# Kernel optimization log

Measured on AMD Instinct MI355X. Metric: run time of the kernel, lower is better.

## Reference

```python
import jax, jax.numpy as jnp
import numpy as np

N, E, F, H, O, B = 100000, 1200000, 64, 1024, 1, 256


def _gcn_conv(x, W, b, src, dst, ew, num_nodes):
    # PyG GCNConv: out_i = sum_{(s->i)} d_i^{-1/2} w_e d_s^{-1/2} (x_s W) + b
    deg = jax.ops.segment_sum(ew, dst, num_segments=num_nodes)
    dinv = jnp.where(deg > 0, jax.lax.rsqrt(jnp.maximum(deg, 1e-12)), 0.0)
    norm = dinv[src] * ew * dinv[dst]          # [E]
    h = x @ W                                   # [N, out]
    msg = h[src] * norm[:, None]                # gather + scale
    return jax.ops.segment_sum(msg, dst, num_segments=num_nodes) + b


def setup_inputs() -> dict:
    key = jax.random.key(0)
    ks = jax.random.split(key, 12)
    def lin(k, fan_in, fan_out):
        s = 1.0 / np.sqrt(fan_in)
        kw, kb = jax.random.split(k)
        return (jax.random.uniform(kw, (fan_in, fan_out), jnp.float32, -s, s),
                jax.random.uniform(kb, (fan_out,), jnp.float32, -s, s))
    W1, b1 = lin(ks[0], F, F)
    W2, b2 = lin(ks[1], F, 2 * F)
    W3, b3 = lin(ks[2], 2 * F, 4 * F)
    Wf1, bf1 = lin(ks[3], 5 * F, H)
    Wf2, bf2 = lin(ks[4], H, O)
    feature = jax.random.normal(ks[5], (N, F), jnp.float32)
    edge_index = jax.random.randint(ks[6], (2, E), 0, N, jnp.int32)
    weight = jax.random.uniform(ks[7], (E,), jnp.float32)
    protein_batch = jnp.sort(jax.random.randint(ks[8], (N,), 0, B, jnp.int32))
    return {"feature": feature, "edge_index": edge_index, "weight": weight,
            "protein_batch": protein_batch,
            "W1": W1, "b1": b1, "W2": W2, "b2": b2, "W3": W3, "b3": b3,
            "Wf1": Wf1, "bf1": bf1, "Wf2": Wf2, "bf2": bf2}


def reference(feature, edge_index, weight, protein_batch,
              W1, b1, W2, b2, W3, b3, Wf1, bf1, Wf2, bf2):
    num_nodes = feature.shape[0]
    # add self-loops with weight 1 (PyG default)
    loop = jnp.arange(num_nodes, dtype=edge_index.dtype)
    src = jnp.concatenate([edge_index[0], loop])
    dst = jnp.concatenate([edge_index[1], loop])
    ew = jnp.concatenate([weight, jnp.ones((num_nodes,), weight.dtype)])

    x = jax.nn.relu(_gcn_conv(feature, W1, b1, src, dst, ew, num_nodes))
    x = jax.nn.relu(_gcn_conv(x, W2, b2, src, dst, ew, num_nodes))
    x = jax.nn.relu(_gcn_conv(x, W3, b3, src, dst, ew, num_nodes))
    x = jnp.concatenate([x, feature], axis=1)   # [N, 5F]

    # global_mean_pool over graph ids
    sums = jax.ops.segment_sum(x, protein_batch, num_segments=B)
    cnts = jax.ops.segment_sum(jnp.ones((num_nodes,), x.dtype), protein_batch, num_segments=B)
    gc = sums / jnp.maximum(cnts, 1.0)[:, None]

    gc = jax.nn.relu(gc @ Wf1 + bf1)            # dropout is identity in eval
    return gc @ Wf2 + bf2
```

## Files before the change

kernel.cpp:

```cpp
#include <hip/hip_runtime.h>
#include <cstdio>
#include <cstdint>

typedef _Float16 f16x8 __attribute__((ext_vector_type(8)));
typedef float f32x4 __attribute__((ext_vector_type(4)));

__device__ inline unsigned short f2bf(float f) {
  unsigned u = __float_as_uint(f);
  u += 0x7fffu + ((u >> 16) & 1u);
  return (unsigned short)(u >> 16);
}
__device__ inline float bf2f(unsigned short h) {
  return __uint_as_float(((unsigned)h) << 16);
}
__device__ inline unsigned short f2h(float f) {
  union { _Float16 h; unsigned short u; } cv;
  cv.h = (_Float16)f;
  return cv.u;
}

#define EPB 8192


__global__ __launch_bounds__(256)
void k_prep0(float* __restrict__ psum,
             const float* __restrict__ feature, ushort* __restrict__ featb,
             const float* __restrict__ W1, ushort* __restrict__ w1h,
             const float* __restrict__ W2, ushort* __restrict__ w2h,
             const float* __restrict__ W3, ushort* __restrict__ w3h,
             const int* __restrict__ pb, int* __restrict__ gs,
             const int* __restrict__ dst, int* __restrict__ H,
             int* __restrict__ rs,
             int BC, int NF, int F, int D2, int D3,
             int N, int B, int NB, int E,
             int nB, int nC, int nD, int nG) {
  __shared__ int hist[512];
  int b = blockIdx.x;
  int t = threadIdx.x;
  if (b < nB) {
    int i = b * 256 + t;
    if (i < BC) psum[i] = 0.f;
  } else if (b < nB + nC) {
    int base = ((b - nB) * 256 + t) * 4;
    if (base < NF) {
      float4 v = *reinterpret_cast<const float4*>(feature + base);
      ushort4 h;
      h.x = f2bf(v.x); h.y = f2bf(v.y); h.z = f2bf(v.z); h.w = f2bf(v.w);
      *reinterpret_cast<ushort4*>(featb + base) = h;
    }
  } else if (b < nB + nC + nD) {
    int idx = (b - nB - nC) * 256 + t;
    int s1 = F * F, s2 = s1 + F * D2, s3 = s2 + D2 * D3;
    if (idx < s1) {
      int k = idx / F, n = idx - k * F;
      w1h[(size_t)n * F + k] = f2h(W1[idx]);
    } else if (idx < s2) {
      int i2 = idx - s1; int k = i2 / D2, n = i2 - k * D2;
      w2h[(size_t)n * F + k] = f2h(W2[i2]);
    } else if (idx < s3) {
      int i3 = idx - s2; int k = i3 / D3, n = i3 - k * D3;
      w3h[(size_t)n * D2 + k] = f2h(W3[i3]);
    }
  } else if (b < nB + nC + nD + nG) {
    int bb = (b - nB - nC - nD) * 256 + t;
    if (bb == 0) rs[N] = E;
    if (bb <= B) {
      int lo = 0, hi = N;
      while (lo < hi) {
        int mid = (lo + hi) >> 1;
        if (pb[mid] < bb) lo = mid + 1; else hi = mid;
      }
      gs[bb] = lo;
    }
  } else {
    const int bi = b - nB - nC - nD - nG;
    for (int i = t; i < NB; i += 256) hist[i] = 0;
    __syncthreads();
    const int base = bi * EPB + t;
#pragma unroll
    for (int j = 0; j < EPB / 256; j++) {
      int e = base + 256 * j;
      if (e < E) atomicAdd(&hist[dst[e] >> 8], 1);
    }
    __syncthreads();
    for (int i = t; i < NB; i += 256) H[(size_t)bi * NB + i] = hist[i];
  }
}

__global__ __launch_bounds__(256)
void k_bscan1(const int* __restrict__ H, int* __restrict__ S,
              int* __restrict__ bsum, int NB, int NBLK, int T) {
  __shared__ int sh[256];
  const int t = threadIdx.x;
  const int base = blockIdx.x * 1024;
  int v[4]; int s = 0;
#pragma unroll
  for (int j = 0; j < 4; j++) {
    int idx = base + t * 4 + j;
    if (idx < T) {
      int bin = idx / NBLK, bi = idx - bin * NBLK;
      v[j] = H[(size_t)bi * NB + bin];
    } else v[j] = 0;
    s += v[j];
  }
  sh[t] = s;
  __syncthreads();
  for (int off = 1; off < 256; off <<= 1) {
    int x = (t >= off) ? sh[t - off] : 0;
    __syncthreads();
    sh[t] += x;
    __syncthreads();
  }
  int run = sh[t] - s;
#pragma unroll
  for (int j = 0; j < 4; j++) {
    int idx = base + t * 4 + j;
    if (idx < T) S[idx] = run;
    run += v[j];
  }
  if (t == 255) bsum[blockIdx.x] = sh[255];
}

__device__ inline void build_prefix(const int* __restrict__ bsum, int nch,
                                    int* __restrict__ pre, int t) {
  for (int i = t; i < nch; i += 256) pre[i] = bsum[i];
  __syncthreads();
  if (t == 0) {
    int run = 0;
    for (int i = 0; i < nch; i++) { int v = pre[i]; pre[i] = run; run += v; }
  }
  __syncthreads();
}

__global__ __launch_bounds__(256)
void k_bscatter(const int* __restrict__ src, const int* __restrict__ dst,
                const float* __restrict__ ew, const int* __restrict__ S,
                const int* __restrict__ bsb,
                int2* __restrict__ ssw,
                int NB, int NBLK, int E, int nchT) {
  __shared__ int cnt[512];
  __shared__ int sbase[512];
  __shared__ int pre[512];
  const int t = threadIdx.x, bi = blockIdx.x;
  build_prefix(bsb, nchT, pre, t);
  for (int i = t; i < NB; i += 256) {
    cnt[i] = 0;
    int j = i * NBLK + bi;
    sbase[i] = S[j] + pre[j >> 10];
  }
  __syncthreads();
  const int base = bi * EPB + t;
#pragma unroll
  for (int j = 0; j < EPB / 256; j++) {
    int e = base + 256 * j;
    if (e < E) {
      int d = dst[e];
      int bin = d >> 8;
      int r = atomicAdd(&cnt[bin], 1);
      int pos = sbase[bin] + r;
      ssw[pos] = make_int2(src[e] | ((d & 255) << 24), __float_as_int(ew[e]));
    }
  }
}

__global__ __launch_bounds__(256)
void k_bprocA(const int2* __restrict__ ssw,
              const int* __restrict__ S, const int* __restrict__ bsb,
              int* __restrict__ cntN, float* __restrict__ wsumN,
              int NB, int NBLK, int N, int E, int nchT) {
  __shared__ int cnt[256];
  __shared__ float wsm[256];
  __shared__ int pre[512];
  const int t = threadIdx.x, bin = blockIdx.x;
  build_prefix(bsb, nchT, pre, t);
  cnt[t] = 0; wsm[t] = 0.f;
  __syncthreads();
  int j0 = bin * NBLK;
  const int start = S[j0] + pre[j0 >> 10];
  int end = E;
  if (bin + 1 < NB) { int j1 = (bin + 1) * NBLK; end = S[j1] + pre[j1 >> 10]; }
  for (int p = start + t; p < end; p += 256) {
    int2 sw = ssw[p];
    int ld = (unsigned)sw.x >> 24;
    atomicAdd(&cnt[ld], 1);
    atomicAdd(&wsm[ld], __int_as_float(sw.y));
  }
  __syncthreads();
  int n = bin * 256 + t;
  if (n < N) { cntN[n] = cnt[t]; wsumN[n] = wsm[t]; }
}

__global__ __launch_bounds__(256)
void k_scan1(const int* __restrict__ cntN, const float* __restrict__ wsumN,
             int* __restrict__ rs, int* __restrict__ bsum,
             float* __restrict__ dinv, float* __restrict__ sn, int N) {
  __shared__ int sh[256];
  const int t = threadIdx.x;
  const int base = blockIdx.x * 1024;
  int v[4]; int s = 0;
#pragma unroll
  for (int j = 0; j < 4; j++) {
    int idx = base + t * 4 + j;
    if (idx < N) {
      v[j] = cntN[idx];
      double deg = 1.0 + (double)wsumN[idx];
      float r = (float)(1.0 / sqrt(deg));
      dinv[idx] = r;
      sn[idx] = r * r;
    } else v[j] = 0;
    s += v[j];
  }
  sh[t] = s;
  __syncthreads();
  for (int off = 1; off < 256; off <<= 1) {
    int x = (t >= off) ? sh[t - off] : 0;
    __syncthreads();
    sh[t] += x;
    __syncthreads();
  }
  int run = sh[t] - s;
#pragma unroll
  for (int j = 0; j < 4; j++) {
    int idx = base + t * 4 + j;
    if (idx < N) rs[idx] = run;
    run += v[j];
  }
  if (t == 255) bsum[blockIdx.x] = sh[255];
}

__global__ __launch_bounds__(256)
void k_bprocB(const int2* __restrict__ ssw,
              const int* __restrict__ S, const int* __restrict__ bsb,
              int* __restrict__ rs, const int* __restrict__ bsumN,
              const float* __restrict__ dinv,
              int2* __restrict__ epack,
              int NB, int NBLK, int N, int E, int nchT, int nchN) {
  __shared__ int cnt[256];
  __shared__ float sdv[256];
  __shared__ int srs[256];
  __shared__ int preT[512];
  __shared__ int preN[128];
  const int t = threadIdx.x, bin = blockIdx.x;
  for (int i = t; i < nchT; i += 256) preT[i] = bsb[i];
  for (int i = t; i < nchN; i += 256) preN[i] = bsumN[i];
  __syncthreads();
  if (t == 0) {
    int run = 0;
    for (int i = 0; i < nchT; i++) { int v = preT[i]; preT[i] = run; run += v; }
    run = 0;
    for (int i = 0; i < nchN; i++) { int v = preN[i]; preN[i] = run; run += v; }
  }
  __syncthreads();
  cnt[t] = 0;
  int n = bin * 256 + t;
  sdv[t] = (n < N) ? dinv[n] : 0.f;
  int rabs = 0;
  if (n < N) {
    rabs = rs[n] + preN[n >> 10];
    rs[n] = rabs;
  }
  srs[t] = rabs;
  __syncthreads();
  int j0 = bin * NBLK;
  const int start = S[j0] + preT[j0 >> 10];
  int end = E;
  if (bin + 1 < NB) { int j1 = (bin + 1) * NBLK; end = S[j1] + preT[j1 >> 10]; }
  for (int p = start + t; p < end; p += 256) {
    int2 sw = ssw[p];
    int ld = (unsigned)sw.x >> 24;
    int sidx = sw.x & 0x00FFFFFF;
    int r = atomicAdd(&cnt[ld], 1);
    float w = dinv[sidx] * __int_as_float(sw.y) * sdv[ld];
    epack[srs[ld] + r] = make_int2(sidx, __float_as_int(w));
  }
}


__device__ inline void bf8_fma(const int4 v, float w, float* acc) {
  acc[0] = fmaf(__uint_as_float((unsigned)v.x << 16), w, acc[0]);
  acc[1] = fmaf(__uint_as_float((unsigned)v.x & 0xffff0000u), w, acc[1]);
  acc[2] = fmaf(__uint_as_float((unsigned)v.y << 16), w, acc[2]);
  acc[3] = fmaf(__uint_as_float((unsigned)v.y & 0xffff0000u), w, acc[3]);
  acc[4] = fmaf(__uint_as_float((unsigned)v.z << 16), w, acc[4]);
  acc[5] = fmaf(__uint_as_float((unsigned)v.z & 0xffff0000u), w, acc[5]);
  acc[6] = fmaf(__uint_as_float((unsigned)v.w << 16), w, acc[6]);
  acc[7] = fmaf(__uint_as_float((unsigned)v.w & 0xffff0000u), w, acc[7]);
}

template<int LOG2L>
__global__ __launch_bounds__(256)
void k_aggregate_b(const ushort* __restrict__ Xb, const int* __restrict__ rs,
                   const int2* __restrict__ epack, const float* __restrict__ sn,
                   ushort* __restrict__ AH, int N) {
  const int t = blockIdx.x * blockDim.x + threadIdx.x;
  const int row = t >> LOG2L;
  if (row >= N) return;
  const int L = 1 << LOG2L;
  const int D = L << 3;
  const int c = (t & (L - 1)) << 3;
  const ushort* __restrict__ Xc = Xb + c;

  float acc[8];
  {
    int4 v = *reinterpret_cast<const int4*>(Xc + (size_t)row * D);
    float s = sn[row];
    acc[0] = s * __uint_as_float((unsigned)v.x << 16);
    acc[1] = s * __uint_as_float((unsigned)v.x & 0xffff0000u);
    acc[2] = s * __uint_as_float((unsigned)v.y << 16);
    acc[3] = s * __uint_as_float((unsigned)v.y & 0xffff0000u);
    acc[4] = s * __uint_as_float((unsigned)v.z << 16);
    acc[5] = s * __uint_as_float((unsigned)v.z & 0xffff0000u);
    acc[6] = s * __uint_as_float((unsigned)v.w << 16);
    acc[7] = s * __uint_as_float((unsigned)v.w & 0xffff0000u);
  }
  const int p0 = rs[row], pe = rs[row + 1];
  int i = p0;
  if ((i & 1) && i < pe) {
    int2 e = epack[i];
    int4 v = *reinterpret_cast<const int4*>(Xc + (size_t)e.x * D);
    bf8_fma(v, __int_as_float(e.y), acc);
    i++;
  }
  for (; i + 8 <= pe; i += 8) {
    int4 ea = *reinterpret_cast<const int4*>(&epack[i]);
    int4 eb = *reinterpret_cast<const int4*>(&epack[i + 2]);
    int4 ec = *reinterpret_cast<const int4*>(&epack[i + 4]);
    int4 ed = *reinterpret_cast<const int4*>(&epack[i + 6]);
    int4 v0 = *reinterpret_cast<const int4*>(Xc + (size_t)ea.x * D);
    int4 v1 = *reinterpret_cast<const int4*>(Xc + (size_t)ea.z * D);
    int4 v2 = *reinterpret_cast<const int4*>(Xc + (size_t)eb.x * D);
    int4 v3 = *reinterpret_cast<const int4*>(Xc + (size_t)eb.z * D);
    int4 v4 = *reinterpret_cast<const int4*>(Xc + (size_t)ec.x * D);
    int4 v5 = *reinterpret_cast<const int4*>(Xc + (size_t)ec.z * D);
    int4 v6 = *reinterpret_cast<const int4*>(Xc + (size_t)ed.x * D);
    int4 v7 = *reinterpret_cast<const int4*>(Xc + (size_t)ed.z * D);
    bf8_fma(v0, __int_as_float(ea.y), acc);
    bf8_fma(v1, __int_as_float(ea.w), acc);
    bf8_fma(v2, __int_as_float(eb.y), acc);
    bf8_fma(v3, __int_as_float(eb.w), acc);
    bf8_fma(v4, __int_as_float(ec.y), acc);
    bf8_fma(v5, __int_as_float(ec.w), acc);
    bf8_fma(v6, __int_as_float(ed.y), acc);
    bf8_fma(v7, __int_as_float(ed.w), acc);
  }
  if (i + 4 <= pe) {
    int4 ea = *reinterpret_cast<const int4*>(&epack[i]);
    int4 eb = *reinterpret_cast<const int4*>(&epack[i + 2]);
    int4 v0 = *reinterpret_cast<const int4*>(Xc + (size_t)ea.x * D);
    int4 v1 = *reinterpret_cast<const int4*>(Xc + (size_t)ea.z * D);
    int4 v2 = *reinterpret_cast<const int4*>(Xc + (size_t)eb.x * D);
    int4 v3 = *reinterpret_cast<const int4*>(Xc + (size_t)eb.z * D);
    bf8_fma(v0, __int_as_float(ea.y), acc);
    bf8_fma(v1, __int_as_float(ea.w), acc);
    bf8_fma(v2, __int_as_float(eb.y), acc);
    bf8_fma(v3, __int_as_float(eb.w), acc);
    i += 4;
  }
  if (i + 2 <= pe) {
    int4 e2 = *reinterpret_cast<const int4*>(&epack[i]);
    int4 v0 = *reinterpret_cast<const int4*>(Xc + (size_t)e2.x * D);
    int4 v1 = *reinterpret_cast<const int4*>(Xc + (size_t)e2.z * D);
    bf8_fma(v0, __int_as_float(e2.y), acc);
    bf8_fma(v1, __int_as_float(e2.w), acc);
    i += 2;
  }
  if (i < pe) {
    int2 e = epack[i];
    int4 v = *reinterpret_cast<const int4*>(Xc + (size_t)e.x * D);
    bf8_fma(v, __int_as_float(e.y), acc);
  }
  ushort h[8];
#pragma unroll
  for (int j = 0; j < 8; j++) h[j] = f2h(acc[j]);
  size_t o = (size_t)row * D + c;
  *reinterpret_cast<ushort4*>(AH + o)     = make_ushort4(h[0], h[1], h[2], h[3]);
  *reinterpret_cast<ushort4*>(AH + o + 4) = make_ushort4(h[4], h[5], h[6], h[7]);
}


template<int KT, int TPB>
__global__ __launch_bounds__(256, 3)
void k_gemm_rb(const ushort* __restrict__ Ah, const ushort* __restrict__ Bh,
               const float* __restrict__ bias, ushort* __restrict__ Y,
               int N, int D) {
  constexpr int NT = 64;
  constexpr int NK = KT / 32;
  const int t = threadIdx.x;
  const int wave = t >> 6, lane = t & 63;
  const int quad = lane >> 4, l16 = lane & 15;
  const int n0 = blockIdx.x * NT;
  const int mbase = blockIdx.y * (TPB * 128);

  f16x8 bf[NK][4];
#pragma unroll
  for (int k0 = 0; k0 < NK; k0++)
#pragma unroll
    for (int ni = 0; ni < 4; ni++)
      bf[k0][ni] = *reinterpret_cast<const f16x8*>(
          Bh + (size_t)(n0 + ni * 16 + l16) * KT + k0 * 32 + quad * 8);

  float bv[4];
#pragma unroll
  for (int ni = 0; ni < 4; ni++) bv[ni] = bias[n0 + ni * 16 + l16];

#pragma unroll 1
  for (int tile = 0; tile < TPB; tile++) {
    const int rt = mbase + tile * 128 + wave * 32 + l16;
    if (mbase + tile * 128 >= N) break;
    int r0 = rt;      if (r0 >= N) r0 = N - 1;
    int r1 = rt + 16; if (r1 >= N) r1 = N - 1;
    const ushort* __restrict__ A0 = Ah + (size_t)r0 * KT + quad * 8;
    const ushort* __restrict__ A1 = Ah + (size_t)r1 * KT + quad * 8;

    f16x8 a0[NK], a1[NK];
#pragma unroll
    for (int k0 = 0; k0 < NK; k0++) {
      a0[k0] = *reinterpret_cast<const f16x8*>(A0 + k0 * 32);
      a1[k0] = *reinterpret_cast<const f16x8*>(A1 + k0 * 32);
    }

    f32x4 acc[2][4];
#pragma unroll
    for (int mi = 0; mi < 2; mi++)
#pragma unroll
      for (int ni = 0; ni < 4; ni++) acc[mi][ni] = (f32x4){0.f, 0.f, 0.f, 0.f};

#pragma unroll
    for (int k0 = 0; k0 < NK; k0++)
#pragma unroll
      for (int ni = 0; ni < 4; ni++) {
        acc[0][ni] = __builtin_amdgcn_mfma_f32_16x16x32_f16(a0[k0], bf[k0][ni], acc[0][ni], 0, 0, 0);
        acc[1][ni] = __builtin_amdgcn_mfma_f32_16x16x32_f16(a1[k0], bf[k0][ni], acc[1][ni], 0, 0, 0);
      }

    const int rb0 = mbase + tile * 128 + wave * 32 + quad * 4;
#pragma unroll
    for (int mi = 0; mi < 2; mi++) {
      int rb = rb0 + mi * 16;
#pragma unroll
      for (int ni = 0; ni < 4; ni++) {
        int col = n0 + ni * 16 + l16;
#pragma unroll
        for (int r = 0; r < 4; r++) {
          int row = rb + r;
          if (row < N)
            Y[(size_t)row * D + col] = f2bf(fmaxf(acc[mi][ni][r] + bv[ni], 0.f));
        }
      }
    }
  }
}


#define PSPLIT 4

__global__ void k_pool(const ushort* __restrict__ X3b, const float* __restrict__ feat,
                       const int* __restrict__ gs, float* __restrict__ psum,
                       int D3, int F) {
  const int c = threadIdx.x;
  const int C = D3 + F;
  const int b = blockIdx.y;
  const int sp = blockIdx.x;
  const int s0 = gs[b], e0 = gs[b + 1];
  const int len = e0 - s0;
  if (len <= 0) return;
  const int chunk = (len + PSPLIT - 1) / PSPLIT;
  const int s = s0 + sp * chunk;
  int e = s + chunk; if (e > e0) e = e0;
  if (s >= e) return;
  const int n = e - s;
  float a0 = 0.f, a1 = 0.f, a2 = 0.f, a3 = 0.f;
  float a4 = 0.f, a5 = 0.f, a6 = 0.f, a7 = 0.f;
  if (c < D3) {
    const ushort* p = X3b + (size_t)s * D3 + c;
    int i = 0;
    for (; i + 8 <= n; i += 8) {
      a0 += bf2f(p[0 * (size_t)D3]);
      a1 += bf2f(p[1 * (size_t)D3]);
      a2 += bf2f(p[2 * (size_t)D3]);
      a3 += bf2f(p[3 * (size_t)D3]);
      a4 += bf2f(p[4 * (size_t)D3]);
      a5 += bf2f(p[5 * (size_t)D3]);
      a6 += bf2f(p[6 * (size_t)D3]);
      a7 += bf2f(p[7 * (size_t)D3]);
      p += 8 * (size_t)D3;
    }
    for (; i < n; i++) { a0 += bf2f(*p); p += D3; }
  } else {
    const float* p = feat + (size_t)s * F + (c - D3);
    int i = 0;
    for (; i + 8 <= n; i += 8) {
      a0 += p[0 * (size_t)F];
      a1 += p[1 * (size_t)F];
      a2 += p[2 * (size_t)F];
      a3 += p[3 * (size_t)F];
      a4 += p[4 * (size_t)F];
      a5 += p[5 * (size_t)F];
      a6 += p[6 * (size_t)F];
      a7 += p[7 * (size_t)F];
      p += 8 * (size_t)F;
    }
    for (; i < n; i++) { a0 += *p; p += F; }
  }
  float tot = ((a0 + a1) + (a2 + a3)) + ((a4 + a5) + (a6 + a7));
  atomicAdd(&psum[(size_t)b * C + c], tot);
}


__global__ __launch_bounds__(256)
void k_fc1(const float* __restrict__ psum, const int* __restrict__ gs,
           const float* __restrict__ Wf1, const float* __restrict__ bf1,
           float* __restrict__ hidden, int C, int Hh) {
  const int b = blockIdx.y;
  __shared__ float gcs[384];
  float invc = 1.f / fmaxf((float)(gs[b + 1] - gs[b]), 1.f);
  for (int c = threadIdx.x; c < C; c += 256)
    gcs[c] = psum[(size_t)b * C + c] * invc;
  __syncthreads();
  const int j = blockIdx.x * 256 + threadIdx.x;
  if (j >= Hh) return;
  const float* w = Wf1 + j;
  float a0 = 0.f, a1 = 0.f, a2 = 0.f, a3 = 0.f;
  int c = 0;
  for (; c + 4 <= C; c += 4) {
    a0 = fmaf(gcs[c + 0], w[(size_t)(c + 0) * Hh], a0);
    a1 = fmaf(gcs[c + 1], w[(size_t)(c + 1) * Hh], a1);
    a2 = fmaf(gcs[c + 2], w[(size_t)(c + 2) * Hh], a2);
    a3 = fmaf(gcs[c + 3], w[(size_t)(c + 3) * Hh], a3);
  }
  for (; c < C; c++) a0 = fmaf(gcs[c], w[(size_t)c * Hh], a0);
  float r = ((a0 + a1) + (a2 + a3)) + bf1[j];
  hidden[(size_t)b * Hh + j] = fmaxf(r, 0.f);
}

__global__ void k_fc2(const float* __restrict__ hidden, const float* __restrict__ Wf2,
                      const float* __restrict__ bf2, float* __restrict__ out, int Hh) {
  int b = blockIdx.x;
  int lane = threadIdx.x;
  double s = 0.0;
  for (int j = lane; j < Hh; j += 64) s += (double)hidden[(size_t)b * Hh + j] * (double)Wf2[j];
#pragma unroll
  for (int off = 32; off > 0; off >>= 1) s += __shfl_down(s, off);
  if (lane == 0) out[b] = (float)s + bf2[0];
}


extern "C" void kernel_launch(void* const* d_in, const int* in_sizes, int n_in,
                              void* d_out, int out_size, void* d_ws, size_t ws_size,
                              hipStream_t stream) {
  const float* feature = (const float*)d_in[0];
  const int*   eidx    = (const int*)  d_in[1];
  const float* weight  = (const float*)d_in[2];
  const int*   pb      = (const int*)  d_in[3];
  const float* W1  = (const float*)d_in[4];
  const float* b1  = (const float*)d_in[5];
  const float* W2  = (const float*)d_in[6];
  const float* b2  = (const float*)d_in[7];
  const float* W3  = (const float*)d_in[8];
  const float* b3  = (const float*)d_in[9];
  const float* Wf1 = (const float*)d_in[10];
  const float* bf1 = (const float*)d_in[11];
  const float* Wf2 = (const float*)d_in[12];
  const float* bf2 = (const float*)d_in[13];

  const int F  = in_sizes[5];
  const int D2 = in_sizes[7];
  const int D3 = in_sizes[9];
  const int Hh = in_sizes[11];
  const int N  = in_sizes[0] / F;
  const int E  = in_sizes[1] / 2;
  const int B  = out_size;
  const int C  = D3 + F;

  const int* srcp = eidx;
  const int* dstp = eidx + E;

  const int NB   = (N + 255) / 256;
  const int NBLK = (E + EPB - 1) / EPB;
  const int T    = NB * NBLK;
  const int nchT = (T + 1023) / 1024;
  const int nchN = (N + 1023) / 1024;

  auto al = [](size_t x) { return (x + 255) & ~(size_t)255; };
  size_t off = 0;
  auto alloc = [&](size_t bytes) { size_t o = off; off += al(bytes); return o; };
  size_t o_H     = alloc((size_t)T * 4);
  size_t o_S     = alloc((size_t)T * 4);
  size_t o_bsb   = alloc((size_t)nchT * 4);
  size_t o_ssw   = alloc((size_t)E * 8);
  size_t o_cntN  = alloc((size_t)N * 4);
  size_t o_wsumN = alloc((size_t)N * 4);
  size_t o_dinv  = alloc((size_t)N * 4);
  size_t o_sn    = alloc((size_t)N * 4);
  size_t o_rs    = alloc((size_t)(N + 1) * 4);
  size_t o_bsum  = alloc((size_t)nchN * 4);
  size_t o_epack = alloc((size_t)E * 8);
  size_t o_featb = alloc((size_t)N * F  * 2);
  size_t o_x1b   = alloc((size_t)N * F  * 2);
  size_t o_x2b   = alloc((size_t)N * D2 * 2);
  size_t o_x3b   = alloc((size_t)N * D3 * 2);
  size_t o_aggh  = alloc((size_t)N * D2 * 2);
  size_t o_w1h   = alloc((size_t)F  * F  * 2);
  size_t o_w2h   = alloc((size_t)F  * D2 * 2);
  size_t o_w3h   = alloc((size_t)D2 * D3 * 2);
  size_t o_psum  = alloc((size_t)B * C * 4);
  size_t o_gs    = alloc((size_t)(B + 1) * 4);
  size_t o_hid   = alloc((size_t)B * Hh * 4);
  if (off > ws_size) {
    fprintf(stderr, "kernel_launch: workspace too small: need %zu, have %zu\n", off, ws_size);
    return;
  }

  char* ws = (char*)d_ws;
  int*    H     = (int*)  (ws + o_H);
  int*    S     = (int*)  (ws + o_S);
  int*    bsb   = (int*)  (ws + o_bsb);
  int2*   ssw   = (int2*) (ws + o_ssw);
  int*    cntN  = (int*)  (ws + o_cntN);
  float*  wsumN = (float*)(ws + o_wsumN);
  float*  dinv  = (float*)(ws + o_dinv);
  float*  sn    = (float*)(ws + o_sn);
  int*    rs    = (int*)  (ws + o_rs);
  int*    bsum  = (int*)  (ws + o_bsum);
  int2*   epack = (int2*) (ws + o_epack);
  ushort* featb = (ushort*)(ws + o_featb);
  ushort* x1b   = (ushort*)(ws + o_x1b);
  ushort* x2b   = (ushort*)(ws + o_x2b);
  ushort* x3b   = (ushort*)(ws + o_x3b);
  ushort* aggh  = (ushort*)(ws + o_aggh);
  ushort* w1h   = (ushort*)(ws + o_w1h);
  ushort* w2h   = (ushort*)(ws + o_w2h);
  ushort* w3h   = (ushort*)(ws + o_w3h);
  float*  psum  = (float*) (ws + o_psum);
  int*    gs    = (int*)  (ws + o_gs);
  float*  hid   = (float*)(ws + o_hid);
  float*  out   = (float*)d_out;

  const int BC = B * C, NF = N * F;
  const int nB = (BC + 255) / 256;
  const int nC = (NF / 4 + 255) / 256;
  const int nD = (F * F + F * D2 + D2 * D3 + 255) / 256;
  const int nG = (B + 1 + 255) / 256;
  k_prep0<<<nB + nC + nD + nG + NBLK, 256, 0, stream>>>(
      psum, feature, featb, W1, w1h, W2, w2h, W3, w3h,
      pb, gs, dstp, H, rs,
      BC, NF, F, D2, D3, N, B, NB, E, nB, nC, nD, nG);

  k_bscan1  <<<nchT, 256, 0, stream>>>(H, S, bsb, NB, NBLK, T);
  k_bscatter<<<NBLK, 256, 0, stream>>>(srcp, dstp, weight, S, bsb, ssw, NB, NBLK, E, nchT);
  k_bprocA  <<<NB, 256, 0, stream>>>(ssw, S, bsb, cntN, wsumN, NB, NBLK, N, E, nchT);
  k_scan1   <<<nchN, 256, 0, stream>>>(cntN, wsumN, rs, bsum, dinv, sn, N);
  k_bprocB  <<<NB, 256, 0, stream>>>(ssw, S, bsb, rs, bsum, dinv, epack, NB, NBLK, N, E, nchT, nchN);

  const int Mt = (N + 127) / 128;

  {
    int tot = N * (F / 8);
    k_aggregate_b<3><<<(tot + 255) / 256, 256, 0, stream>>>(featb, rs, epack, sn, aggh, N);
    dim3 g(1, Mt);
    k_gemm_rb<64, 1><<<g, 256, 0, stream>>>(aggh, w1h, b1, x1b, N, F);
  }
  {
    int tot = N * (F / 8);
    k_aggregate_b<3><<<(tot + 255) / 256, 256, 0, stream>>>(x1b, rs, epack, sn, aggh, N);
    dim3 g(2, (Mt + 1) / 2);
    k_gemm_rb<64, 2><<<g, 256, 0, stream>>>(aggh, w2h, b2, x2b, N, D2);
  }
  {
    int tot = N * (D2 / 8);
    k_aggregate_b<4><<<(tot + 255) / 256, 256, 0, stream>>>(x2b, rs, epack, sn, aggh, N);
    dim3 g(4, (Mt + 3) / 4);
    k_gemm_rb<128, 4><<<g, 256, 0, stream>>>(aggh, w3h, b3, x3b, N, D3);
  }

  {
    dim3 g(PSPLIT, B);
    k_pool<<<g, C, 0, stream>>>(x3b, feature, gs, psum, D3, F);
  }
  {
    dim3 g((Hh + 255) / 256, B);
    k_fc1<<<g, 256, 0, stream>>>(psum, gs, Wf1, bf1, hid, C, Hh);
  }
  k_fc2  <<<B, 64, 0, stream>>>(hid, Wf2, bf2, out, Hh);
}
```

Baseline: 388.1 us.

## Compute per-node degree with global atomics in histogram pass, merge scans

```diff
diff --git a/kernel.cpp b/kernel.cpp
--- a/kernel.cpp
+++ b/kernel.cpp
@@ -29,8 +29,9 @@
              const float* __restrict__ W2, ushort* __restrict__ w2h,
              const float* __restrict__ W3, ushort* __restrict__ w3h,
              const int* __restrict__ pb, int* __restrict__ gs,
-             const int* __restrict__ dst, int* __restrict__ H,
-             int* __restrict__ rs,
+             const int* __restrict__ dst, const float* __restrict__ ew,
+             int* __restrict__ H, int* __restrict__ rs,
+             int* __restrict__ cntN, float* __restrict__ wsumN,
              int BC, int NF, int F, int D2, int D3,
              int N, int B, int NB, int E,
              int nB, int nC, int nD, int nG) {
@@ -80,45 +81,88 @@
 #pragma unroll
     for (int j = 0; j < EPB / 256; j++) {
       int e = base + 256 * j;
-      if (e < E) atomicAdd(&hist[dst[e] >> 8], 1);
+      if (e < E) {
+        int d = dst[e];
+        atomicAdd(&hist[d >> 8], 1);
+        atomicAdd(&cntN[d], 1);
+        atomicAdd(&wsumN[d], ew[e]);
+      }
     }
     __syncthreads();
     for (int i = t; i < NB; i += 256) H[(size_t)bi * NB + i] = hist[i];
   }
 }
 
+
 __global__ __launch_bounds__(256)
-void k_bscan1(const int* __restrict__ H, int* __restrict__ S,
-              int* __restrict__ bsum, int NB, int NBLK, int T) {
+void k_scans(const int* __restrict__ H, int* __restrict__ S,
+             int* __restrict__ bsb,
+             const int* __restrict__ cntN, const float* __restrict__ wsumN,
+             int* __restrict__ rs, int* __restrict__ bsum,
+             float* __restrict__ dinv, float* __restrict__ sn,
+             int NB, int NBLK, int T, int N, int nchT) {
   __shared__ int sh[256];
   const int t = threadIdx.x;
-  const int base = blockIdx.x * 1024;
-  int v[4]; int s = 0;
-#pragma unroll
-  for (int j = 0; j < 4; j++) {
-    int idx = base + t * 4 + j;
-    if (idx < T) {
-      int bin = idx / NBLK, bi = idx - bin * NBLK;
-      v[j] = H[(size_t)bi * NB + bin];
-    } else v[j] = 0;
-    s += v[j];
-  }
-  sh[t] = s;
-  __syncthreads();
-  for (int off = 1; off < 256; off <<= 1) {
-    int x = (t >= off) ? sh[t - off] : 0;
+  if ((int)blockIdx.x < nchT) {
+    const int base = blockIdx.x * 1024;
+    int v[4]; int s = 0;
+#pragma unroll
+    for (int j = 0; j < 4; j++) {
+      int idx = base + t * 4 + j;
+      if (idx < T) {
+        int bin = idx / NBLK, bi = idx - bin * NBLK;
+        v[j] = H[(size_t)bi * NB + bin];
+      } else v[j] = 0;
+      s += v[j];
+    }
+    sh[t] = s;
     __syncthreads();
-    sh[t] += x;
+    for (int off = 1; off < 256; off <<= 1) {
+      int x = (t >= off) ? sh[t - off] : 0;
+      __syncthreads();
+      sh[t] += x;
+      __syncthreads();
+    }
+    int run = sh[t] - s;
+#pragma unroll
+    for (int j = 0; j < 4; j++) {
+      int idx = base + t * 4 + j;
+      if (idx < T) S[idx] = run;
+      run += v[j];
+    }
+    if (t == 255) bsb[blockIdx.x] = sh[255];
+  } else {
+    const int base = (blockIdx.x - nchT) * 1024;
+    int v[4]; int s = 0;
+#pragma unroll
+    for (int j = 0; j < 4; j++) {
+      int idx = base + t * 4 + j;
+      if (idx < N) {
+        v[j] = cntN[idx];
+        double deg = 1.0 + (double)wsumN[idx];
+        float r = (float)(1.0 / sqrt(deg));
+        dinv[idx] = r;
+        sn[idx] = r * r;
+      } else v[j] = 0;
+      s += v[j];
+    }
+    sh[t] = s;
     __syncthreads();
-  }
-  int run = sh[t] - s;
-#pragma unroll
-  for (int j = 0; j < 4; j++) {
-    int idx = base + t * 4 + j;
-    if (idx < T) S[idx] = run;
-    run += v[j];
-  }
-  if (t == 255) bsum[blockIdx.x] = sh[255];
+    for (int off = 1; off < 256; off <<= 1) {
+      int x = (t >= off) ? sh[t - off] : 0;
+      __syncthreads();
+      sh[t] += x;
+      __syncthreads();
+    }
+    int run = sh[t] - s;
+#pragma unroll
+    for (int j = 0; j < 4; j++) {
+      int idx = base + t * 4 + j;
+      if (idx < N) rs[idx] = run;
+      run += v[j];
+    }
+    if (t == 255) bsum[blockIdx.x - nchT] = sh[255];
+  }
 }
 
 __device__ inline void build_prefix(const int* __restrict__ bsum, int nch,
@@ -161,71 +205,6 @@
       ssw[pos] = make_int2(src[e] | ((d & 255) << 24), __float_as_int(ew[e]));
     }
   }
-}
-
-__global__ __launch_bounds__(256)
-void k_bprocA(const int2* __restrict__ ssw,
-              const int* __restrict__ S, const int* __restrict__ bsb,
-              int* __restrict__ cntN, float* __restrict__ wsumN,
-              int NB, int NBLK, int N, int E, int nchT) {
-  __shared__ int cnt[256];
-  __shared__ float wsm[256];
-  __shared__ int pre[512];
-  const int t = threadIdx.x, bin = blockIdx.x;
-  build_prefix(bsb, nchT, pre, t);
-  cnt[t] = 0; wsm[t] = 0.f;
-  __syncthreads();
-  int j0 = bin * NBLK;
-  const int start = S[j0] + pre[j0 >> 10];
-  int end = E;
-  if (bin + 1 < NB) { int j1 = (bin + 1) * NBLK; end = S[j1] + pre[j1 >> 10]; }
-  for (int p = start + t; p < end; p += 256) {
-    int2 sw = ssw[p];
-    int ld = (unsigned)sw.x >> 24;
-    atomicAdd(&cnt[ld], 1);
-    atomicAdd(&wsm[ld], __int_as_float(sw.y));
-  }
-  __syncthreads();
-  int n = bin * 256 + t;
-  if (n < N) { cntN[n] = cnt[t]; wsumN[n] = wsm[t]; }
-}
-
-__global__ __launch_bounds__(256)
-void k_scan1(const int* __restrict__ cntN, const float* __restrict__ wsumN,
-             int* __restrict__ rs, int* __restrict__ bsum,
-             float* __restrict__ dinv, float* __restrict__ sn, int N) {
-  __shared__ int sh[256];
-  const int t = threadIdx.x;
-  const int base = blockIdx.x * 1024;
-  int v[4]; int s = 0;
-#pragma unroll
-  for (int j = 0; j < 4; j++) {
-    int idx = base + t * 4 + j;
-    if (idx < N) {
-      v[j] = cntN[idx];
-      double deg = 1.0 + (double)wsumN[idx];
-      float r = (float)(1.0 / sqrt(deg));
-      dinv[idx] = r;
-      sn[idx] = r * r;
-    } else v[j] = 0;
-    s += v[j];
-  }
-  sh[t] = s;
-  __syncthreads();
-  for (int off = 1; off < 256; off <<= 1) {
-    int x = (t >= off) ? sh[t - off] : 0;
-    __syncthreads();
-    sh[t] += x;
-    __syncthreads();
-  }
-  int run = sh[t] - s;
-#pragma unroll
-  for (int j = 0; j < 4; j++) {
-    int idx = base + t * 4 + j;
-    if (idx < N) rs[idx] = run;
-    run += v[j];
-  }
-  if (t == 255) bsum[blockIdx.x] = sh[255];
 }
 
 __global__ __launch_bounds__(256)
@@ -588,8 +567,7 @@
   size_t o_S     = alloc((size_t)T * 4);
   size_t o_bsb   = alloc((size_t)nchT * 4);
   size_t o_ssw   = alloc((size_t)E * 8);
-  size_t o_cntN  = alloc((size_t)N * 4);
-  size_t o_wsumN = alloc((size_t)N * 4);
+  size_t o_cw    = alloc((size_t)2 * N * 4);
   size_t o_dinv  = alloc((size_t)N * 4);
   size_t o_sn    = alloc((size_t)N * 4);
   size_t o_rs    = alloc((size_t)(N + 1) * 4);
@@ -616,8 +594,8 @@
   int*    S     = (int*)  (ws + o_S);
   int*    bsb   = (int*)  (ws + o_bsb);
   int2*   ssw   = (int2*) (ws + o_ssw);
-  int*    cntN  = (int*)  (ws + o_cntN);
-  float*  wsumN = (float*)(ws + o_wsumN);
+  int*    cntN  = (int*)  (ws + o_cw);
+  float*  wsumN = (float*)(ws + o_cw + (size_t)N * 4);
   float*  dinv  = (float*)(ws + o_dinv);
   float*  sn    = (float*)(ws + o_sn);
   int*    rs    = (int*)  (ws + o_rs);
@@ -636,6 +614,8 @@
   float*  hid   = (float*)(ws + o_hid);
   float*  out   = (float*)d_out;
 
+  hipMemsetAsync(ws + o_cw, 0, (size_t)2 * N * 4, stream);
+
   const int BC = B * C, NF = N * F;
   const int nB = (BC + 255) / 256;
   const int nC = (NF / 4 + 255) / 256;
@@ -643,13 +623,13 @@
   const int nG = (B + 1 + 255) / 256;
   k_prep0<<<nB + nC + nD + nG + NBLK, 256, 0, stream>>>(
       psum, feature, featb, W1, w1h, W2, w2h, W3, w3h,
-      pb, gs, dstp, H, rs,
+      pb, gs, dstp, weight, H, rs, cntN, wsumN,
       BC, NF, F, D2, D3, N, B, NB, E, nB, nC, nD, nG);
 
-  k_bscan1  <<<nchT, 256, 0, stream>>>(H, S, bsb, NB, NBLK, T);
+  k_scans<<<nchT + nchN, 256, 0, stream>>>(
+      H, S, bsb, cntN, wsumN, rs, bsum, dinv, sn, NB, NBLK, T, N, nchT);
+
   k_bscatter<<<NBLK, 256, 0, stream>>>(srcp, dstp, weight, S, bsb, ssw, NB, NBLK, E, nchT);
-  k_bprocA  <<<NB, 256, 0, stream>>>(ssw, S, bsb, cntN, wsumN, NB, NBLK, N, E, nchT);
-  k_scan1   <<<nchN, 256, 0, stream>>>(cntN, wsumN, rs, bsum, dinv, sn, N);
   k_bprocB  <<<NB, 256, 0, stream>>>(ssw, S, bsb, rs, bsum, dinv, epack, NB, NBLK, N, E, nchT, nchN);
 
   const int Mt = (N + 127) / 128;
```

Measured after the change: 537.8 us. 38.6% more time.
